# Optimization experiments

Measured on AMD Instinct MI355X. Metric: run time of the kernel, lower is better.

The kernel has to match this reference:

```python
import jax, jax.numpy as jnp
import numpy as np

B, T, D, H, C = 256, 512, 300, 128, 6

def setup_inputs() -> dict:
    key = jax.random.key(0)
    ks = jax.random.split(key, 8)
    s = 1.0 / np.sqrt(H)  # PyTorch LSTM/Linear uniform init scale
    x = jax.random.normal(ks[0], (B, T, D), dtype=jnp.float32)
    lengths = jax.random.randint(ks[1], (B,), 1, T + 1)
    W_ih = jax.random.uniform(ks[2], (4 * H, D), minval=-s, maxval=s, dtype=jnp.float32)
    W_hh = jax.random.uniform(ks[3], (4 * H, H), minval=-s, maxval=s, dtype=jnp.float32)
    b_ih = jax.random.uniform(ks[4], (4 * H,), minval=-s, maxval=s, dtype=jnp.float32)
    b_hh = jax.random.uniform(ks[5], (4 * H,), minval=-s, maxval=s, dtype=jnp.float32)
    fc_w = jax.random.uniform(ks[6], (C, H), minval=-s, maxval=s, dtype=jnp.float32)
    fc_b = jax.random.uniform(ks[7], (C,), minval=-s, maxval=s, dtype=jnp.float32)
    return {"x": x, "W_ih": W_ih, "W_hh": W_hh, "b_ih": b_ih, "b_hh": b_hh,
            "fc_w": fc_w, "fc_b": fc_b, "lengths": lengths}

def _lstm_last_hidden(x, W_ih, W_hh, b_ih, b_hh, lengths):
    # Equivalent to pack_padded_sequence + nn.LSTM: the returned hidden[-1]
    # is the state at t = length-1 for each sequence. We run a masked scan:
    # state updates are frozen once t >= length.
    Bv, Tv, _ = x.shape
    Hv = W_hh.shape[1]
    xs = jnp.swapaxes(x, 0, 1)                              # [T, B, D]
    gx = jnp.einsum('tbd,gd->tbg', xs, W_ih) + b_ih + b_hh  # [T, B, 4H]
    mask = (jnp.arange(Tv)[:, None] < lengths[None, :])     # [T, B]

    def step(carry, inp):
        h, c = carry
        g, m = inp
        gates = g + h @ W_hh.T                              # [B, 4H]
        i, f, gg, o = jnp.split(gates, 4, axis=-1)          # PyTorch gate order i,f,g,o
        i = jax.nn.sigmoid(i)
        f = jax.nn.sigmoid(f)
        gg = jnp.tanh(gg)
        o = jax.nn.sigmoid(o)
        c_new = f * c + i * gg
        h_new = o * jnp.tanh(c_new)
        m = m[:, None]
        h = jnp.where(m, h_new, h)
        c = jnp.where(m, c_new, c)
        return (h, c), None

    h0 = jnp.zeros((Bv, Hv), dtype=x.dtype)
    c0 = jnp.zeros((Bv, Hv), dtype=x.dtype)
    (h, c), _ = jax.lax.scan(step, (h0, c0), (gx, mask))
    return h

def reference(x, W_ih, W_hh, b_ih, b_hh, fc_w, fc_b, lengths):
    h = _lstm_last_hidden(x, W_ih, W_hh, b_ih, b_hh, lengths)  # [B, H]
    return h @ fc_w.T + fc_b                                   # [B, 6]
```

## Files before the change

kernel.cpp:

```cpp
#include <hip/hip_runtime.h>
#include <hip/hip_bf16.h>
#include <stdint.h>
#include <type_traits>

#define NB 256
#define NT 512
#define ND 300
#define NH 128
#define NG 512
#define NC 6

typedef __attribute__((ext_vector_type(8))) short short8;
typedef __attribute__((ext_vector_type(4))) float f32x4;

static __device__ __forceinline__ float bf2f(unsigned int u) {
  return __builtin_bit_cast(float, (u & 0xffffu) << 16);
}
static __device__ __forceinline__ unsigned short f2bf(float f) {
  return __builtin_bit_cast(unsigned short, __float2bfloat16(f));
}
static __device__ __forceinline__ unsigned int packbf(float a, float b) {
  return (unsigned int)f2bf(a) | ((unsigned int)f2bf(b) << 16);
}
static __device__ __forceinline__ float ld1(const unsigned short* p) { return bf2f(*p); }
static __device__ __forceinline__ float ld1(const float* p) { return *p; }
static __device__ __forceinline__ void st1(unsigned short* p, float v) { *p = f2bf(v); }
static __device__ __forceinline__ void st1(float* p, float v) { *p = v; }

static __device__ __forceinline__ float sigmoid_fast(float x) {
  return __builtin_amdgcn_rcpf(1.f + __expf(-x));
}
static __device__ __forceinline__ float tanh_fast(float x) {
  return 1.f - 2.f * __builtin_amdgcn_rcpf(__expf(2.f * x) + 1.f);
}

#define BARRIER_LGKM() asm volatile("s_waitcnt lgkmcnt(0)\n\ts_barrier" ::: "memory")

static __device__ __forceinline__ uint2 load4bf_fast(const unsigned short* row, int k) {
  return *(const uint2*)(row + k);
}
static __device__ __forceinline__ uint2 load4bf_fast(const float* row, int k) {
  float4 f = *(const float4*)(row + k);
  uint2 v;
  v.x = packbf(f.x, f.y);
  v.y = packbf(f.z, f.w);
  return v;
}
static __device__ __forceinline__ uint2 load4bf(const unsigned short* row, int k, int lim) {
  if (k + 3 < lim) return load4bf_fast(row, k);
  unsigned int e0 = (k + 0 < lim) ? row[k + 0] : 0;
  unsigned int e1 = (k + 1 < lim) ? row[k + 1] : 0;
  unsigned int e2 = (k + 2 < lim) ? row[k + 2] : 0;
  unsigned int e3 = (k + 3 < lim) ? row[k + 3] : 0;
  uint2 v;
  v.x = e0 | (e1 << 16);
  v.y = e2 | (e3 << 16);
  return v;
}
static __device__ __forceinline__ uint2 load4bf(const float* row, int k, int lim) {
  if (k + 3 < lim) return load4bf_fast(row, k);
  float f0 = (k + 0 < lim) ? row[k + 0] : 0.f;
  float f1 = (k + 1 < lim) ? row[k + 1] : 0.f;
  float f2 = (k + 2 < lim) ? row[k + 2] : 0.f;
  float f3 = (k + 3 < lim) ? row[k + 3] : 0.f;
  uint2 v;
  v.x = packbf(f0, f1);
  v.y = packbf(f2, f3);
  return v;
}

__global__ void detect_dtype(const unsigned short* __restrict__ X, int* __restrict__ flag) {
  __shared__ int cnt;
  if (threadIdx.x == 0) cnt = 0;
  __syncthreads();
  int c = 0;
  for (int i = threadIdx.x; i < 512; i += 64) {
    unsigned int u = X[i];
    unsigned int e = (u >> 7) & 0xffu;
    if (u == 0u || (e >= 97u && e <= 157u)) c++;
  }
  atomicAdd(&cnt, c);
  __syncthreads();
  if (threadIdx.x == 0) *flag = (cnt >= 448) ? 0 : 1;
}

template <typename XT, typename GXT>
__global__ __launch_bounds__(256) void gx_gemm(const int* __restrict__ flag, int want,
                                               const XT* __restrict__ X,
                                               const XT* __restrict__ Wih,
                                               const XT* __restrict__ bih,
                                               const XT* __restrict__ bhh,
                                               const int* __restrict__ lengths,
                                               GXT* __restrict__ gx,
                                               int b_base, int t_base, int Tc) {
  if (*flag != want) return;
  const int mb = blockIdx.x;
  const int m0 = mb << 6;
  const int bc = m0 / Tc;
  const int trel0 = m0 % Tc;
  const int b = b_base + bc;
  const int t0 = t_base + trel0;
  const int len = lengths[b];
  if (t0 >= len) return;

  __shared__ unsigned short As[10][64][40];
  __shared__ unsigned short Bs[2][128][40];

  const int tid = threadIdx.x;
  const int lane = tid & 63;
  const int wave = tid >> 6;
  const int wm = wave & 1;
  const int wn = wave >> 1;
  const int lq = lane >> 4;
  const int lr = lane & 15;

  const int rA = tid >> 2;
  const int cA = (tid & 3) << 2;
  const XT* xrow = X + ((size_t)b * NT + t0 + rA) * ND;
  {
    uint2 a0[10], a1[10];
#pragma unroll
    for (int kc = 0; kc < 9; ++kc) {
      a0[kc] = load4bf_fast(xrow, kc * 32 + cA);
      a1[kc] = load4bf_fast(xrow, kc * 32 + 16 + cA);
    }
    a0[9] = load4bf(xrow, 288 + cA, ND);
    a1[9] = load4bf(xrow, 288 + 16 + cA, ND);
#pragma unroll
    for (int kc = 0; kc < 10; ++kc) {
      *(uint2*)&As[kc][rA][cA] = a0[kc];
      *(uint2*)&As[kc][rA][16 + cA] = a1[kc];
    }
  }

  const int rb = tid >> 3;
  const int kq = tid & 7;

  uint2 bv[3][4];
  {
    const XT* wb = Wih + (size_t)rb * ND;
#pragma unroll
    for (int s3 = 0; s3 < 3; ++s3)
#pragma unroll
      for (int j = 0; j < 4; ++j)
        bv[s3][j] = load4bf_fast(wb + (size_t)(32 * j) * ND, s3 * 32 + kq * 4);
  }

  for (int nt = 0; nt < 4; ++nt) {
    const int n0 = nt << 7;
    const XT* wb = Wih + (size_t)(n0 + rb) * ND;

    f32x4 acc[2][4];
#pragma unroll
    for (int i = 0; i < 2; ++i)
#pragma unroll
      for (int j = 0; j < 4; ++j) {
        f32x4 z = {0.f, 0.f, 0.f, 0.f};
        acc[i][j] = z;
      }

#pragma unroll
    for (int j = 0; j < 4; ++j) *(uint2*)&Bs[0][rb + 32 * j][kq * 4] = bv[0][j];
    BARRIER_LGKM();

#pragma unroll
    for (int kc = 0; kc < 10; ++kc) {
      const int bi = kc & 1;
      if (kc < 9) {
#pragma unroll
        for (int j = 0; j < 4; ++j)
          *(uint2*)&Bs[bi ^ 1][rb + 32 * j][kq * 4] = bv[(kc + 1) % 3][j];
      }
      if (kc < 7) {
        const int kn = (kc + 3) * 32 + kq * 4;
        if (kc < 6) {
#pragma unroll
          for (int j = 0; j < 4; ++j)
            bv[kc % 3][j] = load4bf_fast(wb + (size_t)(32 * j) * ND, kn);
        } else {
#pragma unroll
          for (int j = 0; j < 4; ++j)
            bv[kc % 3][j] = load4bf(wb + (size_t)(32 * j) * ND, kn, ND);
        }
      }

      short8 af[2], bq[4];
#pragma unroll
      for (int tm = 0; tm < 2; ++tm)
        af[tm] = *(const short8*)&As[kc][wm * 32 + tm * 16 + lr][lq * 8];
#pragma unroll
      for (int tn = 0; tn < 4; ++tn)
        bq[tn] = *(const short8*)&Bs[bi][wn * 64 + tn * 16 + lr][lq * 8];
#pragma unroll
      for (int tm = 0; tm < 2; ++tm)
#pragma unroll
        for (int tn = 0; tn < 4; ++tn)
          acc[tm][tn] =
              __builtin_amdgcn_mfma_f32_16x16x32_bf16(af[tm], bq[tn], acc[tm][tn], 0, 0, 0);
      BARRIER_LGKM();
    }

    if (nt < 3) {
      const XT* wb2 = Wih + (size_t)((nt + 1) * 128 + rb) * ND;
#pragma unroll
      for (int s3 = 0; s3 < 3; ++s3)
#pragma unroll
        for (int j = 0; j < 4; ++j)
          bv[s3][j] = load4bf_fast(wb2 + (size_t)(32 * j) * ND, s3 * 32 + kq * 4);
    }

    float bias_c[4];
#pragma unroll
    for (int tn = 0; tn < 4; ++tn) {
      const int col = n0 + wn * 64 + tn * 16 + lr;
      bias_c[tn] = ld1(bih + col) + ld1(bhh + col);
    }
#pragma unroll
    for (int tm = 0; tm < 2; ++tm)
#pragma unroll
      for (int tn = 0; tn < 4; ++tn)
#pragma unroll
        for (int rg = 0; rg < 4; ++rg) {
          const int row = wm * 32 + tm * 16 + lq * 4 + rg;
          if (t0 + row < len) {
            const int col = n0 + wn * 64 + tn * 16 + lr;
            st1(gx + (size_t)(m0 + row) * NG + col, acc[tm][tn][rg] + bias_c[tn]);
          }
        }
  }
}

template <typename XT, typename GXT>
__global__ __launch_bounds__(512)
__attribute__((amdgpu_waves_per_eu(2, 2)))
void lstm_rec(const int* __restrict__ flag, int want,
              const GXT* __restrict__ gx,
              const XT* __restrict__ Whh,
              const XT* __restrict__ fcw,
              const XT* __restrict__ fcb,
              const int* __restrict__ lengths,
              XT* __restrict__ out,
              float* __restrict__ hstate,
              float* __restrict__ cstate,
              int b_base, int t_base, int Tc) {
  if (*flag != want) return;
  const int bc = blockIdx.x;
  const int b = b_base + bc;
  int len = lengths[b];
  if (len > NT) len = NT;
  if (len < 0) len = 0;
  const bool first = (t_base == 0);
  const bool last = (t_base + Tc >= NT);
  const int tend = (len < t_base + Tc) ? len : (t_base + Tc);
  if (!last && tend <= t_base) return;
  int nsteps = tend - t_base;
  if (nsteps < 0) nsteps = 0;

  const int tid = threadIdx.x;
  const int w8 = tid >> 6;
  const int l = tid & 63;
  const int q = l >> 4;
  const int m = l & 15;
  const int u0 = w8 * 16 + q * 4;
  const int r = m & 3;
  const int u = u0 + r;

  __shared__ __align__(16) unsigned short hpk[2][NH];
  __shared__ __align__(16) float hf[NH];

  short8 afr[4][4];
#pragma unroll
  for (int g = 0; g < 4; ++g) {
    const int row = g * NH + w8 * 16 + m;
    if constexpr (std::is_same_v<XT, unsigned short>) {
#pragma unroll
      for (int c = 0; c < 4; ++c)
        afr[g][c] = *(const short8*)(Whh + (size_t)row * NH + c * 32 + q * 8);
    } else {
#pragma unroll
      for (int c = 0; c < 4; ++c) {
        const float* p = Whh + (size_t)row * NH + c * 32 + q * 8;
        float4 f0 = *(const float4*)p;
        float4 f1 = *(const float4*)(p + 4);
        union { unsigned int uu[4]; short8 s; } cv2;
        cv2.uu[0] = packbf(f0.x, f0.y);
        cv2.uu[1] = packbf(f0.z, f0.w);
        cv2.uu[2] = packbf(f1.x, f1.y);
        cv2.uu[3] = packbf(f1.z, f1.w);
        afr[g][c] = cv2.s;
      }
    }
  }

  float hcur = 0.f, ccur = 0.f;
  if (!first) {
    hcur = hstate[(size_t)bc * NH + u];
    ccur = cstate[(size_t)bc * NH + u];
  }
  if (m < 4) hpk[0][u] = f2bf(hcur);
  __syncthreads();

  const GXT* gp = gx + (size_t)bc * Tc * NG + u;
  const int lastidx = (nsteps > 0) ? nsteps - 1 : 0;

  float gs0[4], gs1[4];
  {
    const int i1 = (1 < lastidx) ? 1 : lastidx;
#pragma unroll
    for (int g = 0; g < 4; ++g) {
      gs0[g] = ld1(gp + g * NH);
      gs1[g] = ld1(gp + (size_t)i1 * NG + g * NH);
    }
  }

#define REC_STEP(S, PAR, GC)                                                         \
  {                                                                                  \
    short8 bfr[4];                                                                   \
    const unsigned short* hrow = hpk[(PAR)];                                         \
    _Pragma("unroll") for (int c = 0; c < 4; ++c)                                    \
        bfr[c] = *(const short8*)&hrow[c * 32 + q * 8];                              \
    f32x4 acc[4];                                                                    \
    _Pragma("unroll") for (int g = 0; g < 4; ++g) {                                  \
      f32x4 z = {0.f, 0.f, 0.f, 0.f};                                                \
      acc[g] = z;                                                                    \
      _Pragma("unroll") for (int c = 0; c < 4; ++c)                                  \
          acc[g] = __builtin_amdgcn_mfma_f32_16x16x32_bf16(afr[g][c], bfr[c],        \
                                                           acc[g], 0, 0, 0);         \
    }                                                                                \
    float pre[4];                                                                    \
    _Pragma("unroll") for (int g = 0; g < 4; ++g) {                                  \
      const float t0v = (r & 1) ? acc[g][1] : acc[g][0];                             \
      const float t1v = (r & 1) ? acc[g][3] : acc[g][2];                             \
      pre[g] = ((r & 2) ? t1v : t0v) + GC[g];                                        \
    }                                                                                \
    {                                                                                \
      int idx_ = (S) + 2;                                                            \
      if (idx_ > lastidx) idx_ = lastidx;                                            \
      _Pragma("unroll") for (int g = 0; g < 4; ++g)                                  \
          GC[g] = ld1(gp + (size_t)idx_ * NG + g * NH);                              \
    }                                                                                \
    const float ig = sigmoid_fast(pre[0]);                                           \
    const float fg = sigmoid_fast(pre[1]);                                           \
    const float gg = tanh_fast(pre[2]);                                              \
    const float og = sigmoid_fast(pre[3]);                                           \
    ccur = fmaf(fg, ccur, ig * gg);                                                  \
    hcur = og * tanh_fast(ccur);                                                     \
    if (m < 4) hpk[(PAR) ^ 1][u] = f2bf(hcur);                                       \
    BARRIER_LGKM();                                                                  \
  }

  int s = 0;
  for (; s + 1 < nsteps; s += 2) {
    REC_STEP(s, 0, gs0);
    REC_STEP(s + 1, 1, gs1);
  }
  if (s < nsteps) {
    REC_STEP(s, 0, gs0);
  }
#undef REC_STEP

  if (!last) {
    if (m < 4) {
      hstate[(size_t)bc * NH + u] = hcur;
      cstate[(size_t)bc * NH + u] = ccur;
    }
  } else {
    if (m < 4) hf[u] = hcur;
    __syncthreads();
    if (tid < NC) {
      float acc = ld1(fcb + tid);
      const XT* wv = fcw + (size_t)tid * NH;
#pragma unroll
      for (int k = 0; k < NH; ++k) acc = fmaf(ld1(wv + k), hf[k], acc);
      st1(out + (size_t)b * NC + tid, acc);
    }
  }
}

template <typename XT, typename GXT>
static void run_variant(int want, const int* flag, void* const* d_in, XT* out,
                        GXT* gx, float* hstate, float* cstate, int NBc, int Tc,
                        hipStream_t stream) {
  const XT* X = (const XT*)d_in[0];
  const XT* Wih = (const XT*)d_in[1];
  const XT* Whh = (const XT*)d_in[2];
  const XT* bih = (const XT*)d_in[3];
  const XT* bhh = (const XT*)d_in[4];
  const XT* fcw = (const XT*)d_in[5];
  const XT* fcb = (const XT*)d_in[6];
  const int* lengths = (const int*)d_in[7];
  for (int bb = 0; bb < NB; bb += NBc) {
    for (int tb = 0; tb < NT; tb += Tc) {
      gx_gemm<XT, GXT><<<dim3((NBc * Tc) / 64), dim3(256), 0, stream>>>(
          flag, want, X, Wih, bih, bhh, lengths, gx, bb, tb, Tc);
      lstm_rec<XT, GXT><<<dim3(NBc), dim3(512), 0, stream>>>(
          flag, want, gx, Whh, fcw, fcb, lengths, out, hstate, cstate, bb, tb, Tc);
    }
  }
}

extern "C" void kernel_launch(void* const* d_in, const int* in_sizes, int n_in,
                              void* d_out, int out_size, void* d_ws, size_t ws_size,
                              hipStream_t stream) {
  int* flag = (int*)d_ws;
  detect_dtype<<<dim3(1), dim3(64), 0, stream>>>((const unsigned short*)d_in[0], flag);

  const size_t full_f32 = (size_t)NB * NT * NG * sizeof(float);
  const size_t full_bf16 = (size_t)NB * NT * NG * 2;
  const size_t base = 512;

  int NBc, Tc;
  char* gx_raw;
  float* hstate = (float*)((char*)d_ws + base);
  bool gx_is_f32;

  if (ws_size >= base + full_f32) {
    NBc = NB; Tc = NT; gx_is_f32 = true;
    gx_raw = (char*)d_ws + base;
  } else if (ws_size >= base + full_bf16) {
    NBc = NB; Tc = NT; gx_is_f32 = false;
    gx_raw = (char*)d_ws + base;
  } else {
    Tc = 128; gx_is_f32 = false;
    NBc = 1;
    for (int cand : {64, 16, 4}) {
      size_t need = base + (size_t)cand * NH * 2 * sizeof(float) + (size_t)cand * Tc * NG * 2;
      if (ws_size >= need) { NBc = cand; break; }
    }
    gx_raw = (char*)d_ws + base + (size_t)NBc * NH * 2 * sizeof(float);
  }
  float* cstate = hstate + (size_t)NBc * NH;

  if (gx_is_f32) {
    run_variant<unsigned short, float>(0, flag, d_in, (unsigned short*)d_out,
                                       (float*)gx_raw, hstate, cstate, NBc, Tc, stream);
    run_variant<float, float>(1, flag, d_in, (float*)d_out, (float*)gx_raw, hstate,
                              cstate, NBc, Tc, stream);
  } else {
    run_variant<unsigned short, unsigned short>(0, flag, d_in, (unsigned short*)d_out,
                                                (unsigned short*)gx_raw, hstate, cstate,
                                                NBc, Tc, stream);
    run_variant<float, unsigned short>(1, flag, d_in, (float*)d_out,
                                       (unsigned short*)gx_raw, hstate, cstate, NBc, Tc,
                                       stream);
  }
}
```

Measured before the change: 583.8 us.

## Detect dtype inside kernels and halve launch count; split MFMA accumulation chains

Removes the separate dtype-detection kernel and the duplicated per-dtype launch sequence. Each gemm and recurrence block now inspects the input itself and branches to the float or bf16 body, so only one set of kernels is launched. The recurrent gate MFMAs are also made independent (four products summed afterwards) instead of a serial accumulate chain, which shortens the per-step dependency latency. The cost is that every block repeats the small detection read plus a shared-memory reduction, and both bodies sit in one kernel, which may raise register pressure.

After: 710.3 us. 21.7% more time.

```diff
diff --git a/kernel.cpp b/kernel.cpp
--- a/kernel.cpp
+++ b/kernel.cpp
@@ -69,31 +69,32 @@
   return v;
 }
 
-__global__ void detect_dtype(const unsigned short* __restrict__ X, int* __restrict__ flag) {
-  __shared__ int cnt;
-  if (threadIdx.x == 0) cnt = 0;
+static __device__ __forceinline__ int block_detect(const unsigned short* __restrict__ X,
+                                                   int* cnt) {
+  const int tid = threadIdx.x;
+  const int nthr = blockDim.x;
+  if (tid == 0) *cnt = 0;
   __syncthreads();
   int c = 0;
-  for (int i = threadIdx.x; i < 512; i += 64) {
+  for (int i = tid; i < 512; i += nthr) {
     unsigned int u = X[i];
     unsigned int e = (u >> 7) & 0xffu;
     if (u == 0u || (e >= 97u && e <= 157u)) c++;
   }
-  atomicAdd(&cnt, c);
+  if (c) atomicAdd(cnt, c);
   __syncthreads();
-  if (threadIdx.x == 0) *flag = (cnt >= 448) ? 0 : 1;
+  return (*cnt >= 448) ? 0 : 1;
 }
 
 template <typename XT, typename GXT>
-__global__ __launch_bounds__(256) void gx_gemm(const int* __restrict__ flag, int want,
-                                               const XT* __restrict__ X,
-                                               const XT* __restrict__ Wih,
-                                               const XT* __restrict__ bih,
-                                               const XT* __restrict__ bhh,
-                                               const int* __restrict__ lengths,
-                                               GXT* __restrict__ gx,
-                                               int b_base, int t_base, int Tc) {
-  if (*flag != want) return;
+static __device__ __forceinline__ void gx_body(
+    const XT* __restrict__ X, const XT* __restrict__ Wih,
+    const XT* __restrict__ bih, const XT* __restrict__ bhh,
+    const int* __restrict__ lengths, GXT* __restrict__ gx,
+    int b_base, int t_base, int Tc, unsigned short* smem) {
+  auto As = reinterpret_cast<unsigned short(*)[64][40]>(smem);
+  auto Bs = reinterpret_cast<unsigned short(*)[128][40]>(smem + 25600);
+
   const int mb = blockIdx.x;
   const int m0 = mb << 6;
   const int bc = m0 / Tc;
@@ -103,9 +104,6 @@
   const int len = lengths[b];
   if (t0 >= len) return;
 
-  __shared__ unsigned short As[10][64][40];
-  __shared__ unsigned short Bs[2][128][40];
-
   const int tid = threadIdx.x;
   const int lane = tid & 63;
   const int wave = tid >> 6;
@@ -231,19 +229,13 @@
 }
 
 template <typename XT, typename GXT>
-__global__ __launch_bounds__(512)
-__attribute__((amdgpu_waves_per_eu(2, 2)))
-void lstm_rec(const int* __restrict__ flag, int want,
-              const GXT* __restrict__ gx,
-              const XT* __restrict__ Whh,
-              const XT* __restrict__ fcw,
-              const XT* __restrict__ fcb,
-              const int* __restrict__ lengths,
-              XT* __restrict__ out,
-              float* __restrict__ hstate,
-              float* __restrict__ cstate,
-              int b_base, int t_base, int Tc) {
-  if (*flag != want) return;
+static __device__ __forceinline__ void rec_body(
+    const GXT* __restrict__ gx, const XT* __restrict__ Whh,
+    const XT* __restrict__ fcw, const XT* __restrict__ fcb,
+    const int* __restrict__ lengths, XT* __restrict__ out,
+    float* __restrict__ hstate, float* __restrict__ cstate,
+    int b_base, int t_base, int Tc,
+    unsigned short (*hpk)[NH], float* hf) {
   const int bc = blockIdx.x;
   const int b = b_base + bc;
   int len = lengths[b];
@@ -265,9 +257,6 @@
   const int r = m & 3;
   const int u = u0 + r;
 
-  __shared__ __align__(16) unsigned short hpk[2][NH];
-  __shared__ __align__(16) float hf[NH];
-
   short8 afr[4][4];
 #pragma unroll
   for (int g = 0; g < 4; ++g) {
@@ -319,13 +308,14 @@
     const unsigned short* hrow = hpk[(PAR)];                                         \
     _Pragma("unroll") for (int c = 0; c < 4; ++c)                                    \
         bfr[c] = *(const short8*)&hrow[c * 32 + q * 8];                              \
+    const f32x4 zz = {0.f, 0.f, 0.f, 0.f};                                           \
     f32x4 acc[4];                                                                    \
     _Pragma("unroll") for (int g = 0; g < 4; ++g) {                                  \
-      f32x4 z = {0.f, 0.f, 0.f, 0.f};                                                \
-      acc[g] = z;                                                                    \
-      _Pragma("unroll") for (int c = 0; c < 4; ++c)                                  \
-          acc[g] = __builtin_amdgcn_mfma_f32_16x16x32_bf16(afr[g][c], bfr[c],        \
-                                                           acc[g], 0, 0, 0);         \
+      f32x4 p0 = __builtin_amdgcn_mfma_f32_16x16x32_bf16(afr[g][0], bfr[0], zz, 0, 0, 0); \
+      f32x4 p1 = __builtin_amdgcn_mfma_f32_16x16x32_bf16(afr[g][1], bfr[1], zz, 0, 0, 0); \
+      f32x4 p2 = __builtin_amdgcn_mfma_f32_16x16x32_bf16(afr[g][2], bfr[2], zz, 0, 0, 0); \
+      f32x4 p3 = __builtin_amdgcn_mfma_f32_16x16x32_bf16(afr[g][3], bfr[3], zz, 0, 0, 0); \
+      acc[g] = (p0 + p1) + (p2 + p3);                                                \
     }                                                                                \
     float pre[4];                                                                    \
     _Pragma("unroll") for (int g = 0; g < 4; ++g) {                                  \
@@ -377,24 +367,61 @@
   }
 }
 
-template <typename XT, typename GXT>
-static void run_variant(int want, const int* flag, void* const* d_in, XT* out,
-                        GXT* gx, float* hstate, float* cstate, int NBc, int Tc,
-                        hipStream_t stream) {
-  const XT* X = (const XT*)d_in[0];
-  const XT* Wih = (const XT*)d_in[1];
-  const XT* Whh = (const XT*)d_in[2];
-  const XT* bih = (const XT*)d_in[3];
-  const XT* bhh = (const XT*)d_in[4];
-  const XT* fcw = (const XT*)d_in[5];
-  const XT* fcb = (const XT*)d_in[6];
+template <typename GXT>
+__global__ __launch_bounds__(256) void gx_gemm_rt(const void* __restrict__ X,
+                                                  const void* __restrict__ Wih,
+                                                  const void* __restrict__ bih,
+                                                  const void* __restrict__ bhh,
+                                                  const int* __restrict__ lengths,
+                                                  GXT* __restrict__ gx,
+                                                  int b_base, int t_base, int Tc) {
+  __shared__ int cnt;
+  __shared__ __align__(16) unsigned short smem[35840];
+  const int isf32 = block_detect((const unsigned short*)X, &cnt);
+  if (isf32)
+    gx_body<float, GXT>((const float*)X, (const float*)Wih, (const float*)bih,
+                        (const float*)bhh, lengths, gx, b_base, t_base, Tc, smem);
+  else
+    gx_body<unsigned short, GXT>((const unsigned short*)X, (const unsigned short*)Wih,
+                                 (const unsigned short*)bih, (const unsigned short*)bhh,
+                                 lengths, gx, b_base, t_base, Tc, smem);
+}
+
+template <typename GXT>
+__global__ __launch_bounds__(512)
+__attribute__((amdgpu_waves_per_eu(2, 2)))
+void lstm_rec_rt(const void* __restrict__ X, const GXT* __restrict__ gx,
+                 const void* __restrict__ Whh, const void* __restrict__ fcw,
+                 const void* __restrict__ fcb, const int* __restrict__ lengths,
+                 void* __restrict__ out, float* __restrict__ hstate,
+                 float* __restrict__ cstate, int b_base, int t_base, int Tc) {
+  __shared__ int cnt;
+  __shared__ __align__(16) unsigned short hpk[2][NH];
+  __shared__ __align__(16) float hf[NH];
+  const int isf32 = block_detect((const unsigned short*)X, &cnt);
+  if (isf32)
+    rec_body<float, GXT>(gx, (const float*)Whh, (const float*)fcw, (const float*)fcb,
+                         lengths, (float*)out, hstate, cstate, b_base, t_base, Tc,
+                         hpk, hf);
+  else
+    rec_body<unsigned short, GXT>(gx, (const unsigned short*)Whh,
+                                  (const unsigned short*)fcw,
+                                  (const unsigned short*)fcb, lengths,
+                                  (unsigned short*)out, hstate, cstate, b_base,
+                                  t_base, Tc, hpk, hf);
+}
+
+template <typename GXT>
+static void run_all(void* const* d_in, void* d_out, GXT* gx, float* hstate,
+                    float* cstate, int NBc, int Tc, hipStream_t stream) {
   const int* lengths = (const int*)d_in[7];
   for (int bb = 0; bb < NB; bb += NBc) {
     for (int tb = 0; tb < NT; tb += Tc) {
-      gx_gemm<XT, GXT><<<dim3((NBc * Tc) / 64), dim3(256), 0, stream>>>(
-          flag, want, X, Wih, bih, bhh, lengths, gx, bb, tb, Tc);
-      lstm_rec<XT, GXT><<<dim3(NBc), dim3(512), 0, stream>>>(
-          flag, want, gx, Whh, fcw, fcb, lengths, out, hstate, cstate, bb, tb, Tc);
+      gx_gemm_rt<GXT><<<dim3((NBc * Tc) / 64), dim3(256), 0, stream>>>(
+          d_in[0], d_in[1], d_in[3], d_in[4], lengths, gx, bb, tb, Tc);
+      lstm_rec_rt<GXT><<<dim3(NBc), dim3(512), 0, stream>>>(
+          d_in[0], gx, d_in[2], d_in[5], d_in[6], lengths, d_out, hstate, cstate,
+          bb, tb, Tc);
     }
   }
 }
@@ -402,9 +429,6 @@
 extern "C" void kernel_launch(void* const* d_in, const int* in_sizes, int n_in,
                               void* d_out, int out_size, void* d_ws, size_t ws_size,
                               hipStream_t stream) {
-  int* flag = (int*)d_ws;
-  detect_dtype<<<dim3(1), dim3(64), 0, stream>>>((const unsigned short*)d_in[0], flag);
-
   const size_t full_f32 = (size_t)NB * NT * NG * sizeof(float);
   const size_t full_bf16 = (size_t)NB * NT * NG * 2;
   const size_t base = 512;
@@ -432,16 +456,9 @@
   float* cstate = hstate + (size_t)NBc * NH;
 
   if (gx_is_f32) {
-    run_variant<unsigned short, float>(0, flag, d_in, (unsigned short*)d_out,
-                                       (float*)gx_raw, hstate, cstate, NBc, Tc, stream);
-    run_variant<float, float>(1, flag, d_in, (float*)d_out, (float*)gx_raw, hstate,
-                              cstate, NBc, Tc, stream);
+    run_all<float>(d_in, d_out, (float*)gx_raw, hstate, cstate, NBc, Tc, stream);
   } else {
-    run_variant<unsigned short, unsigned short>(0, flag, d_in, (unsigned short*)d_out,
-                                                (unsigned short*)gx_raw, hstate, cstate,
-                                                NBc, Tc, stream);
-    run_variant<float, unsigned short>(1, flag, d_in, (float*)d_out,
-                                       (unsigned short*)gx_raw, hstate, cstate, NBc, Tc,
-                                       stream);
-  }
-}
+    run_all<unsigned short>(d_in, d_out, (unsigned short*)gx_raw, hstate, cstate,
+                            NBc, Tc, stream);
+  }
+}
```
